# Optimization experiments

Measured on AMD Instinct MI355X. Metric: run time of the kernel, lower is better.

The kernel has to match this reference:

```python
import jax, jax.numpy as jnp
import numpy as np

# BERT-base geometry
B, N, H, DH = 4, 512, 12, 64
HID = H * DH            # 768
E = 65536               # total edges (~avg degree 32)
NREL = 64               # relation vocabulary


def setup_inputs() -> dict:
    key = jax.random.key(0)
    ks = jax.random.split(key, 12)
    node_states = jax.random.normal(ks[0], (B, N, HID), jnp.float32)
    b = jax.random.randint(ks[1], (E,), 0, B)
    hn = jax.random.randint(ks[2], (E,), 0, N)
    tn = jax.random.randint(ks[3], (E,), 0, N)
    r = jax.random.randint(ks[4], (E,), 0, NREL)
    edge_indices = jnp.stack([b, hn, tn, r]).astype(jnp.int32)  # (4, E)
    node_type_ids = jnp.zeros((B, N), jnp.int32)  # unused by this subclass
    sc = 0.02
    Wq = jax.random.normal(ks[5], (HID, HID), jnp.float32) * sc
    bq = jnp.zeros((HID,), jnp.float32)
    Wk = jax.random.normal(ks[6], (HID, HID), jnp.float32) * sc
    bk = jnp.zeros((HID,), jnp.float32)
    Wv = jax.random.normal(ks[7], (HID, HID), jnp.float32) * sc
    bv = jnp.zeros((HID,), jnp.float32)
    # relation matrix embeddings: one (DH, DH) matrix per relation id
    rel_emb = jnp.eye(DH, dtype=jnp.float32)[None] + jax.random.normal(ks[8], (NREL, DH, DH), jnp.float32) * sc
    return {"node_states": node_states, "edge_indices": edge_indices,
            "node_type_ids": node_type_ids, "Wq": Wq, "bq": bq,
            "Wk": Wk, "bk": bk, "Wv": Wv, "bv": bv, "rel_emb": rel_emb}


def reference(node_states, edge_indices, node_type_ids, Wq, bq, Wk, bk, Wv, bv, rel_emb):
    Bq, Nn, hid = node_states.shape
    # dense QKV projections (torch Linear: y = x @ W^T + b)
    Q = node_states @ Wq.T + bq
    K = node_states @ Wk.T + bk
    V = (node_states @ Wv.T + bv).reshape(Bq, Nn, H, DH)  # (B,N,H,D)
    be, he, te, re = edge_indices  # each (E,)
    # per-edge gathers
    Qe = Q[be, he].reshape(-1, H, DH)   # (E,H,D)
    Ke = K[be, te].reshape(-1, H, DH)   # (E,H,D)
    Re = rel_emb[re]                     # (E,D,D) relation matrix per edge
    # Q projected through relation matrix, then inner product with K per head
    Qp = jnp.einsum('ehd,edk->ehk', Qe, Re)
    logits = jnp.einsum('ehd,ehd->eh', Qp, Ke) / jnp.sqrt(jnp.float32(DH))  # (E,H)
    # sparse softmax over tail nodes: segment = (batch, head_node)
    seg = be * Nn + he
    nseg = Bq * Nn
    m = jax.ops.segment_max(logits, seg, num_segments=nseg)      # (BN,H)
    ex = jnp.exp(logits - m[seg])
    denom = jax.ops.segment_sum(ex, seg, num_segments=nseg)      # (BN,H)
    p = ex / denom[seg]                                          # (E,H)
    # dropout prob = 0.0 (deterministic reference)
    # aggregate: out[b,i,h,:] = sum_edges p_e * V[b, tail_e, h, :]
    contrib = p[:, :, None] * V[be, te]                          # (E,H,D)
    out = jax.ops.segment_sum(contrib, seg, num_segments=nseg)   # (BN,H,D)
    return out.reshape(Bq, Nn, H * DH)
```

## Files before the change

### kernel.cpp

```cpp
#include <hip/hip_runtime.h>
#include <hip/hip_bf16.h>

#define NB   4
#define NN   512
#define NH   12
#define DHD  64
#define HID  768
#define NE   65536
#define NSEG 2048
#define NREL 64
#define NSUB 32
#define NRSUB (NREL * NSUB)
#define LGS  16

typedef short bf16x8 __attribute__((ext_vector_type(8)));
typedef float f32x4  __attribute__((ext_vector_type(4)));

__device__ __forceinline__ unsigned short f2bf(float f) {
    __hip_bfloat16 h = __float2bfloat16(f);
    return *reinterpret_cast<unsigned short*>(&h);
}
__device__ __forceinline__ float bf2f(unsigned short s) {
    return __int_as_float(((int)s) << 16);
}
__device__ __forceinline__ void load_lds16(const void* g, void* l) {
    __builtin_amdgcn_global_load_lds(
        (const __attribute__((address_space(1))) unsigned int*)g,
        (__attribute__((address_space(3))) unsigned int*)l, 16, 0, 0);
}

#define NX4 ((2048 * 768) / 4)
#define NW4 ((768 * 768) / 4)
__global__ __launch_bounds__(256) void cast_kernel(
    const float* __restrict__ X, const float* __restrict__ Wq,
    const float* __restrict__ Wk, const float* __restrict__ Wv,
    unsigned short* __restrict__ Xh, unsigned short* __restrict__ Wh)
{
    const int i = blockIdx.x * 256 + threadIdx.x;
    float4 v;
    ushort4* dst;
    if (i < NX4) {
        v = ((const float4*)X)[i];
        dst = &((ushort4*)Xh)[i];
    } else {
        const int j = i - NX4;
        const float* W = (j < NW4) ? Wq : ((j < 2 * NW4) ? Wk : Wv);
        const int jj = (j < NW4) ? j : ((j < 2 * NW4) ? j - NW4 : j - 2 * NW4);
        v = ((const float4*)W)[jj];
        dst = &((ushort4*)Wh)[j];
    }
    ushort4 r;
    r.x = f2bf(v.x); r.y = f2bf(v.y); r.z = f2bf(v.z); r.w = f2bf(v.w);
    *dst = r;
}

__global__ __launch_bounds__(256) void qkv_mfma(
    const unsigned short* __restrict__ Xh, const unsigned short* __restrict__ Wh,
    const float* __restrict__ bq, const float* __restrict__ bk,
    const float* __restrict__ bv,
    unsigned short* __restrict__ Qh, unsigned short* __restrict__ Kh,
    float* __restrict__ Vo)
{
    const int z = blockIdx.z;
    const unsigned short* W = Wh + (size_t)z * (768 * 768);
    const float* bias = (z == 0) ? bq : ((z == 1) ? bk : bv);

    const int n0 = blockIdx.x * 128;
    const int m0 = blockIdx.y * 128;
    const int tid  = threadIdx.x;
    const int lane = tid & 63;
    const int wave = tid >> 6;
    const int wm = wave >> 1, wn = wave & 1;

    __shared__ unsigned short As[128 * 64];
    __shared__ unsigned short Bs[128 * 64];

    f32x4 acc[4][4];
    #pragma unroll
    for (int a = 0; a < 4; ++a)
        #pragma unroll
        for (int b = 0; b < 4; ++b) acc[a][b] = (f32x4){0.f, 0.f, 0.f, 0.f};

    const int ml = lane & 15;
    const int q4 = lane >> 4;

    for (int k0 = 0; k0 < HID; k0 += 64) {
        __syncthreads();
        #pragma unroll
        for (int l = 0; l < 4; ++l) {
            const int idx = (l * 4 + wave) * 64 + lane;
            const int row = idx >> 3;
            const int kq  = (idx & 7) ^ (row & 7);
            load_lds16(Xh + (size_t)(m0 + row) * HID + k0 + kq * 8,
                       As + (l * 4 + wave) * 512);
            load_lds16(W + (size_t)(n0 + row) * HID + k0 + kq * 8,
                       Bs + (l * 4 + wave) * 512);
        }
        __syncthreads();

        #pragma unroll
        for (int ks = 0; ks < 2; ++ks) {
            bf16x8 af[4], bfr[4];
            #pragma unroll
            for (int t = 0; t < 4; ++t) {
                const int ar = wm * 64 + t * 16 + ml;
                const int ac = (ks * 4 + q4) ^ (ar & 7);
                af[t] = *(const bf16x8*)(As + ar * 64 + ac * 8);
                const int br = wn * 64 + t * 16 + ml;
                const int bc = (ks * 4 + q4) ^ (br & 7);
                bfr[t] = *(const bf16x8*)(Bs + br * 64 + bc * 8);
            }
            #pragma unroll
            for (int mt = 0; mt < 4; ++mt)
                #pragma unroll
                for (int nt = 0; nt < 4; ++nt)
                    acc[mt][nt] = __builtin_amdgcn_mfma_f32_16x16x32_bf16(
                        af[mt], bfr[nt], acc[mt][nt], 0, 0, 0);
        }
    }

    #pragma unroll
    for (int nt = 0; nt < 4; ++nt) {
        const int col = n0 + wn * 64 + nt * 16 + ml;
        const float bcol = bias[col];
        #pragma unroll
        for (int mt = 0; mt < 4; ++mt) {
            const int row = m0 + wm * 64 + mt * 16 + q4 * 4;
            #pragma unroll
            for (int rg = 0; rg < 4; ++rg) {
                const float v = acc[mt][nt][rg] + bcol;
                const size_t o = (size_t)(row + rg) * HID + col;
                if (z == 0)      Qh[o] = f2bf(v);
                else if (z == 1) Kh[o] = f2bf(v);
                else             Vo[o] = v;
            }
        }
    }
}

__global__ void hist_kernel(const int* __restrict__ ei,
                            int* __restrict__ count, int* __restrict__ rcount2)
{
    const int e = blockIdx.x * 256 + threadIdx.x;
    const int b  = ei[e];
    const int hn = ei[NE + e];
    const int rr = ei[3 * NE + e];
    const int sub = (e >> 8) & (NSUB - 1);
    atomicAdd(&count[b * NN + hn], 1);
    atomicAdd(&rcount2[rr * NSUB + sub], 1);
}

__global__ void scan2_kernel(const int* __restrict__ cntA, int* __restrict__ ofsA,
                             const int* __restrict__ cntB, int* __restrict__ ofsB)
{
    const int* cnt = blockIdx.x ? cntB : cntA;
    int* ofs       = blockIdx.x ? ofsB : ofsA;
    __shared__ int buf[256];
    const int tid = threadIdx.x;
    int local[8];
    int s = 0;
    #pragma unroll
    for (int i = 0; i < 8; ++i) { local[i] = cnt[tid * 8 + i]; s += local[i]; }
    buf[tid] = s;
    __syncthreads();
    for (int off = 1; off < 256; off <<= 1) {
        const int v = (tid >= off) ? buf[tid - off] : 0;
        __syncthreads();
        buf[tid] += v;
        __syncthreads();
    }
    int run = buf[tid] - s;
    #pragma unroll
    for (int i = 0; i < 8; ++i) { ofs[tid * 8 + i] = run; run += local[i]; }
    if (tid == 255) ofs[2048] = run;
}

__global__ void scatter_kernel(const int* __restrict__ ei, const int* __restrict__ offs,
                               int* __restrict__ cursor,
                               const int* __restrict__ rofs2, int* __restrict__ rcursor2,
                               int* __restrict__ s_te, int* __restrict__ s_seg,
                               int* __restrict__ r_pos)
{
    const int e = blockIdx.x * 256 + threadIdx.x;
    const int b  = ei[e];
    const int hn = ei[NE + e];
    const int tn = ei[2 * NE + e];
    const int rr = ei[3 * NE + e];
    const int sub = (e >> 8) & (NSUB - 1);
    const int seg = b * NN + hn;
    const int pos = offs[seg] + atomicAdd(&cursor[seg], 1);
    s_te[pos]  = tn;
    s_seg[pos] = seg;
    const int rb = rr * NSUB + sub;
    const int rj = atomicAdd(&rcursor2[rb], 1);
    r_pos[rofs2[rb] + rj] = pos;
}

#define RLY 32
__global__ __launch_bounds__(256) void rel_logits(
    const unsigned short* __restrict__ Qh, const unsigned short* __restrict__ Kh,
    const float* __restrict__ rel,
    const int* __restrict__ rofs2, const int* __restrict__ r_pos,
    const int* __restrict__ s_te, const int* __restrict__ s_seg,
    float* __restrict__ Lg)
{
    const int r = blockIdx.x;
    const int rstart = rofs2[r * NSUB];
    const int rows = (rofs2[(r + 1) * NSUB] - rstart) * NH;
    const int tid = threadIdx.x;
    const int lane = tid & 63;
    const int wave = tid >> 6;

    __shared__ float ReS[64][65];
    __shared__ int qb[256], kb[256], oi[256];
    __shared__ float QpS[4][16][68];

    {
        const float* Rg = rel + (size_t)r * 4096;
        for (int i = tid; i < 1024; i += 256) {
            const float4 v = ((const float4*)Rg)[i];
            const int row = i >> 4, c4 = (i & 15) * 4;
            ReS[row][c4] = v.x; ReS[row][c4 + 1] = v.y;
            ReS[row][c4 + 2] = v.z; ReS[row][c4 + 3] = v.w;
        }
    }
    __syncthreads();

    bf16x8 bfrag[2][4];
    {
        const int q4 = lane >> 4, n = lane & 15;
        #pragma unroll
        for (int ks = 0; ks < 2; ++ks)
            #pragma unroll
            for (int nt = 0; nt < 4; ++nt) {
                bf16x8 f;
                #pragma unroll
                for (int j = 0; j < 8; ++j)
                    f[j] = (short)f2bf(ReS[ks * 32 + q4 * 8 + j][nt * 16 + n]);
                bfrag[ks][nt] = f;
            }
    }

    for (int t0 = blockIdx.y * 256; t0 < rows; t0 += RLY * 256) {
        __syncthreads();
        {
            const int rowid = t0 + tid;
            if (rowid < rows) {
                const int el = rowid / 12;
                const int h  = rowid - el * 12;
                const int pos = r_pos[rstart + el];
                const int seg = s_seg[pos];
                const int te  = s_te[pos];
                const int b   = seg >> 9;
                qb[tid] = seg * HID + h * 64;
                kb[tid] = (b * NN + te) * HID + h * 64;
                oi[tid] = pos * LGS + h;
            } else { qb[tid] = 0; kb[tid] = 0; oi[tid] = -1; }
        }
        __syncthreads();

        for (int g = wave; g < 16; g += 4) {
            const int m = lane & 15, q4 = lane >> 4;
            const int qbase = qb[g * 16 + m];
            f32x4 cfr[4] = {{0,0,0,0},{0,0,0,0},{0,0,0,0},{0,0,0,0}};
            #pragma unroll
            for (int ks = 0; ks < 2; ++ks) {
                const bf16x8 afr = *(const bf16x8*)(Qh + qbase + ks * 32 + q4 * 8);
                #pragma unroll
                for (int nt = 0; nt < 4; ++nt)
                    cfr[nt] = __builtin_amdgcn_mfma_f32_16x16x32_bf16(
                        afr, bfrag[ks][nt], cfr[nt], 0, 0, 0);
            }
            #pragma unroll
            for (int nt = 0; nt < 4; ++nt)
                #pragma unroll
                for (int rg = 0; rg < 4; ++rg)
                    QpS[wave][q4 * 4 + rg][nt * 16 + m] = cfr[nt][rg];

            const int rw = lane >> 2, ch = (lane & 3) * 16;
            const int rowid2 = g * 16 + rw;
            const int kbase = kb[rowid2];
            const bf16x8 k0 = *(const bf16x8*)(Kh + kbase + ch);
            const bf16x8 k1 = *(const bf16x8*)(Kh + kbase + ch + 8);
            float s = 0.f;
            #pragma unroll
            for (int i = 0; i < 8; ++i) {
                s = fmaf(QpS[wave][rw][ch + i],     bf2f((unsigned short)k0[i]), s);
                s = fmaf(QpS[wave][rw][ch + 8 + i], bf2f((unsigned short)k1[i]), s);
            }
            s += __shfl_xor(s, 1, 64);
            s += __shfl_xor(s, 2, 64);
            if ((lane & 3) == 0) {
                const int o = oi[rowid2];
                if (o >= 0) Lg[o] = s * 0.125f;
            }
        }
    }
}

__global__ __launch_bounds__(256) void seg_softmax_agg(
    const float* __restrict__ V, const float* __restrict__ Lg,
    const int* __restrict__ offs, const int* __restrict__ s_te,
    float* __restrict__ out)
{
    const int seg  = blockIdx.x;
    const int tid  = threadIdx.x;
    const int lane = tid & 63;
    const int w    = tid >> 6;
    const int start = offs[seg];
    const int cnt   = offs[seg + 1] - start;
    const int browbase = seg & ~(NN - 1);

    __shared__ int   te_s[64];
    __shared__ float pv[4][3][64];

    float l0 = 0.f, l1 = 0.f, l2 = 0.f;
    float acc0 = 0.f, acc1 = 0.f, acc2 = 0.f;

    for (int c0 = 0; c0 < cnt; c0 += 64) {
        const int cc = min(64, cnt - c0);
        __syncthreads();
        if (tid < cc) te_s[tid] = s_te[start + c0 + tid];
        __syncthreads();

        float p0 = 0.f, p1 = 0.f, p2 = 0.f;
        if (lane < cc) {
            const float* Lp = Lg + (size_t)(start + c0 + lane) * LGS;
            p0 = __expf(Lp[w]); p1 = __expf(Lp[4 + w]); p2 = __expf(Lp[8 + w]);
        }
        float s0 = p0, s1 = p1, s2 = p2;
        #pragma unroll
        for (int o = 1; o < 64; o <<= 1) {
            s0 += __shfl_xor(s0, o, 64);
            s1 += __shfl_xor(s1, o, 64);
            s2 += __shfl_xor(s2, o, 64);
        }
        l0 += s0; l1 += s1; l2 += s2;
        pv[w][0][lane] = p0; pv[w][1][lane] = p1; pv[w][2][lane] = p2;

        for (int j = 0; j < cc; ++j) {
            const float* __restrict__ Vr =
                V + (size_t)(browbase + te_s[j]) * HID + lane;
            acc0 = fmaf(pv[w][0][j], Vr[w * 64],       acc0);
            acc1 = fmaf(pv[w][1][j], Vr[(4 + w) * 64], acc1);
            acc2 = fmaf(pv[w][2][j], Vr[(8 + w) * 64], acc2);
        }
    }

    float* Yo = out + (size_t)seg * HID;
    Yo[tid]       = (l0 > 0.f) ? acc0 / l0 : 0.f;
    Yo[tid + 256] = (l1 > 0.f) ? acc1 / l1 : 0.f;
    Yo[tid + 512] = (l2 > 0.f) ? acc2 / l2 : 0.f;
}

extern "C" void kernel_launch(void* const* d_in, const int* in_sizes, int n_in,
                              void* d_out, int out_size, void* d_ws, size_t ws_size,
                              hipStream_t stream)
{
    const float* X   = (const float*)d_in[0];
    const int*   EI  = (const int*)d_in[1];
    const float* Wq  = (const float*)d_in[3];
    const float* bq  = (const float*)d_in[4];
    const float* Wk  = (const float*)d_in[5];
    const float* bk  = (const float*)d_in[6];
    const float* Wv  = (const float*)d_in[7];
    const float* bv  = (const float*)d_in[8];
    const float* rel = (const float*)d_in[9];
    float* out = (float*)d_out;

    char* p = (char*)d_ws;
    unsigned short* Qh = (unsigned short*)p;  p += (size_t)NSEG * HID * 2;
    unsigned short* Kh = (unsigned short*)p;  p += (size_t)NSEG * HID * 2;
    float* Vb = (float*)p;                    p += (size_t)NSEG * HID * 4;
    unsigned short* Xh = (unsigned short*)p;
    float* Lg = (float*)p;                    p += (size_t)NE * LGS * 4;
    unsigned short* Wh = (unsigned short*)p;  p += (size_t)3 * 768 * 768 * 2;
    int* offs     = (int*)p;                  p += 2052 * 4;
    int* rofs2    = (int*)p;                  p += (NRSUB + 4) * 4;
    int* count    = (int*)p;                  p += NSEG * 4;
    int* cursor   = (int*)p;                  p += NSEG * 4;
    int* rcount2  = (int*)p;                  p += NRSUB * 4;
    int* rcursor2 = (int*)p;                  p += NRSUB * 4;
    int* s_te     = (int*)p;                  p += NE * 4;
    int* s_seg    = (int*)p;                  p += NE * 4;
    int* r_pos    = (int*)p;                  p += NE * 4;

    cast_kernel<<<(NX4 + 3 * NW4 + 255) / 256, 256, 0, stream>>>(
        X, Wq, Wk, Wv, Xh, Wh);
    qkv_mfma<<<dim3(HID / 128, (NB * NN) / 128, 3), 256, 0, stream>>>(
        Xh, Wh, bq, bk, bv, Qh, Kh, Vb);

    hipMemsetAsync(count, 0, (2 * NSEG + 2 * NRSUB) * sizeof(int), stream);
    hist_kernel<<<NE / 256, 256, 0, stream>>>(EI, count, rcount2);
    scan2_kernel<<<2, 256, 0, stream>>>(count, offs, rcount2, rofs2);
    scatter_kernel<<<NE / 256, 256, 0, stream>>>(EI, offs, cursor, rofs2, rcursor2,
                                                 s_te, s_seg, r_pos);

    rel_logits<<<dim3(NREL, RLY), 256, 0, stream>>>(Qh, Kh, rel, rofs2, r_pos,
                                                    s_te, s_seg, Lg);
    seg_softmax_agg<<<NSEG, 256, 0, stream>>>(Vb, Lg, offs, s_te, out);
}
```

Baseline: 184.0 us.

## Halve QKV GEMM M-tile, stage epilogue through LDS, fuse counter memset

Shrinks the QKV GEMM tile from 128x128 to 64x128, which doubles the block count for better CU occupancy on the small 2048-row GEMM. The accumulators are staged through shared memory so the bias add and stores become vectorized 16-byte writes instead of scattered 2-byte and 4-byte ones. The counter-zeroing memset is folded into the cast kernel, removing one launch. The smaller tile lowers data reuse per block and the epilogue adds extra syncs and LDS traffic.

```diff
diff --git a/kernel.cpp b/kernel.cpp
--- a/kernel.cpp
+++ b/kernel.cpp
@@ -15,6 +15,7 @@
 
 typedef short bf16x8 __attribute__((ext_vector_type(8)));
 typedef float f32x4  __attribute__((ext_vector_type(4)));
+typedef unsigned short u16x8 __attribute__((ext_vector_type(8)));
 
 __device__ __forceinline__ unsigned short f2bf(float f) {
     __hip_bfloat16 h = __float2bfloat16(f);
@@ -34,8 +35,10 @@
 __global__ __launch_bounds__(256) void cast_kernel(
     const float* __restrict__ X, const float* __restrict__ Wq,
     const float* __restrict__ Wk, const float* __restrict__ Wv,
-    unsigned short* __restrict__ Xh, unsigned short* __restrict__ Wh)
-{
+    unsigned short* __restrict__ Xh, unsigned short* __restrict__ Wh,
+    int* __restrict__ counters)
+{
+    if (blockIdx.x < 32) counters[blockIdx.x * 256 + threadIdx.x] = 0;
     const int i = blockIdx.x * 256 + threadIdx.x;
     float4 v;
     ushort4* dst;
@@ -66,18 +69,20 @@
     const float* bias = (z == 0) ? bq : ((z == 1) ? bk : bv);
 
     const int n0 = blockIdx.x * 128;
-    const int m0 = blockIdx.y * 128;
+    const int m0 = blockIdx.y * 64;
     const int tid  = threadIdx.x;
     const int lane = tid & 63;
     const int wave = tid >> 6;
     const int wm = wave >> 1, wn = wave & 1;
 
-    __shared__ unsigned short As[128 * 64];
-    __shared__ unsigned short Bs[128 * 64];
-
-    f32x4 acc[4][4];
+    __shared__ __align__(16) char smem[64 * 132 * 4];
+    unsigned short* As = (unsigned short*)smem;
+    unsigned short* Bs = (unsigned short*)(smem + 8192);
+    float* Cs = (float*)smem;
+
+    f32x4 acc[2][4];
     #pragma unroll
-    for (int a = 0; a < 4; ++a)
+    for (int a = 0; a < 2; ++a)
         #pragma unroll
         for (int b = 0; b < 4; ++b) acc[a][b] = (f32x4){0.f, 0.f, 0.f, 0.f};
 
@@ -87,31 +92,42 @@
     for (int k0 = 0; k0 < HID; k0 += 64) {
         __syncthreads();
         #pragma unroll
-        for (int l = 0; l < 4; ++l) {
-            const int idx = (l * 4 + wave) * 64 + lane;
+        for (int i = 0; i < 2; ++i) {
+            const int slotb = i * 256 + wave * 64;
+            const int idx = slotb + lane;
             const int row = idx >> 3;
             const int kq  = (idx & 7) ^ (row & 7);
             load_lds16(Xh + (size_t)(m0 + row) * HID + k0 + kq * 8,
-                       As + (l * 4 + wave) * 512);
+                       As + slotb * 8);
+        }
+        #pragma unroll
+        for (int i = 0; i < 4; ++i) {
+            const int slotb = i * 256 + wave * 64;
+            const int idx = slotb + lane;
+            const int row = idx >> 3;
+            const int kq  = (idx & 7) ^ (row & 7);
             load_lds16(W + (size_t)(n0 + row) * HID + k0 + kq * 8,
-                       Bs + (l * 4 + wave) * 512);
+                       Bs + slotb * 8);
         }
         __syncthreads();
 
         #pragma unroll
         for (int ks = 0; ks < 2; ++ks) {
-            bf16x8 af[4], bfr[4];
-            #pragma unroll
-            for (int t = 0; t < 4; ++t) {
-                const int ar = wm * 64 + t * 16 + ml;
+            bf16x8 af[2], bfr[4];
+            #pragma unroll
+            for (int t = 0; t < 2; ++t) {
+                const int ar = wm * 32 + t * 16 + ml;
                 const int ac = (ks * 4 + q4) ^ (ar & 7);
                 af[t] = *(const bf16x8*)(As + ar * 64 + ac * 8);
+            }
+            #pragma unroll
+            for (int t = 0; t < 4; ++t) {
                 const int br = wn * 64 + t * 16 + ml;
                 const int bc = (ks * 4 + q4) ^ (br & 7);
                 bfr[t] = *(const bf16x8*)(Bs + br * 64 + bc * 8);
             }
             #pragma unroll
-            for (int mt = 0; mt < 4; ++mt)
+            for (int mt = 0; mt < 2; ++mt)
                 #pragma unroll
                 for (int nt = 0; nt < 4; ++nt)
                     acc[mt][nt] = __builtin_amdgcn_mfma_f32_16x16x32_bf16(
@@ -119,21 +135,45 @@
         }
     }
 
+    __syncthreads();
     #pragma unroll
-    for (int nt = 0; nt < 4; ++nt) {
-        const int col = n0 + wn * 64 + nt * 16 + ml;
-        const float bcol = bias[col];
-        #pragma unroll
-        for (int mt = 0; mt < 4; ++mt) {
-            const int row = m0 + wm * 64 + mt * 16 + q4 * 4;
-            #pragma unroll
-            for (int rg = 0; rg < 4; ++rg) {
-                const float v = acc[mt][nt][rg] + bcol;
-                const size_t o = (size_t)(row + rg) * HID + col;
-                if (z == 0)      Qh[o] = f2bf(v);
-                else if (z == 1) Kh[o] = f2bf(v);
-                else             Vo[o] = v;
-            }
+    for (int mt = 0; mt < 2; ++mt)
+        #pragma unroll
+        for (int nt = 0; nt < 4; ++nt)
+            #pragma unroll
+            for (int rg = 0; rg < 4; ++rg)
+                Cs[(wm * 32 + mt * 16 + q4 * 4 + rg) * 132 +
+                   wn * 64 + nt * 16 + ml] = acc[mt][nt][rg];
+    __syncthreads();
+
+    #pragma unroll
+    for (int it = 0; it < 4; ++it) {
+        const int id  = tid + it * 256;
+        const int row = id >> 4;
+        const int cg  = id & 15;
+        const float* cp = Cs + row * 132 + cg * 8;
+        const float4 cA = *(const float4*)cp;
+        const float4 cB = *(const float4*)(cp + 4);
+        const float* bp = bias + n0 + cg * 8;
+        const float4 bA = *(const float4*)bp;
+        const float4 bB = *(const float4*)(bp + 4);
+        const size_t o = (size_t)(m0 + row) * HID + n0 + cg * 8;
+        if (z == 2) {
+            float4 rA, rB;
+            rA.x = cA.x + bA.x; rA.y = cA.y + bA.y;
+            rA.z = cA.z + bA.z; rA.w = cA.w + bA.w;
+            rB.x = cB.x + bB.x; rB.y = cB.y + bB.y;
+            rB.z = cB.z + bB.z; rB.w = cB.w + bB.w;
+            *(float4*)&Vo[o]     = rA;
+            *(float4*)&Vo[o + 4] = rB;
+        } else {
+            u16x8 r;
+            r[0] = f2bf(cA.x + bA.x); r[1] = f2bf(cA.y + bA.y);
+            r[2] = f2bf(cA.z + bA.z); r[3] = f2bf(cA.w + bA.w);
+            r[4] = f2bf(cB.x + bB.x); r[5] = f2bf(cB.y + bB.y);
+            r[6] = f2bf(cB.z + bB.z); r[7] = f2bf(cB.w + bB.w);
+            unsigned short* Y = (z == 0) ? Qh : Kh;
+            *(u16x8*)&Y[o] = r;
         }
     }
 }
@@ -386,11 +426,10 @@
     int* r_pos    = (int*)p;                  p += NE * 4;
 
     cast_kernel<<<(NX4 + 3 * NW4 + 255) / 256, 256, 0, stream>>>(
-        X, Wq, Wk, Wv, Xh, Wh);
-    qkv_mfma<<<dim3(HID / 128, (NB * NN) / 128, 3), 256, 0, stream>>>(
+        X, Wq, Wk, Wv, Xh, Wh, count);
+    qkv_mfma<<<dim3(HID / 128, (NB * NN) / 64, 3), 256, 0, stream>>>(
         Xh, Wh, bq, bk, bv, Qh, Kh, Vb);
 
-    hipMemsetAsync(count, 0, (2 * NSEG + 2 * NRSUB) * sizeof(int), stream);
     hist_kernel<<<NE / 256, 256, 0, stream>>>(EI, count, rcount2);
     scan2_kernel<<<2, 256, 0, stream>>>(count, offs, rcount2, rofs2);
     scatter_kernel<<<NE / 256, 256, 0, stream>>>(EI, offs, cursor, rofs2, rcursor2,
```

After: 177.7 us. -3.4%, faster.
